# Kernel tuning notes

Measured on AMD Instinct MI355X. Metric: run time of the kernel, lower is better.

Reference implementation:

```python
import jax, jax.numpy as jnp
import numpy as np

V0 = 25; WIN = 3; NS = 6; EPS = 1e-5

def _build_scales():
    # ring graph on 25 joints (matches A_binary in init_kwargs)
    A = np.zeros((V0, V0), np.float32)
    for i in range(V0):
        A[i, (i + 1) % V0] = 1.0; A[(i + 1) % V0, i] = 1.0
    AL = np.tile(A + np.eye(V0, dtype=A.dtype), (WIN, WIN))  # spatial-temporal graph (75x75)
    I = np.eye(len(AL), dtype=AL.dtype)
    def shell(k):
        return np.minimum(np.linalg.matrix_power(AL + I, k), 1) - np.minimum(np.linalg.matrix_power(AL + I, k - 1), 1)
    def kadj(k):
        return I.copy() if k == 0 else shell(k) + I  # with_self=True
    def norm(g):
        dinv = np.power(g.sum(-1), -0.5)
        Dm = np.eye(len(g)) * dinv
        return (Dm @ g @ Dm).astype(np.float32)
    def klap(k):
        if k == 0:
            return I.astype(np.float32)
        Ak = shell(k)
        D = Ak.sum(-1)
        Dm = np.eye(len(D)) * np.power(D, -0.5)
        return (Dm @ (np.eye(len(D)) * (D + 2) - Ak) @ Dm).astype(np.float32)
    A_scales = np.concatenate([norm(kadj(k)) for k in range(NS)])  # (NS*75, 75)
    B_scales = np.concatenate([klap(k) for k in range(NS)])        # (NS*75, 75)
    return jnp.asarray(A_scales), jnp.asarray(B_scales)

def _bn(x, g, b):
    # BatchNorm2d in training mode: batch stats over (N, T, V)
    m = x.mean(axis=(0, 2, 3), keepdims=True)
    v = x.var(axis=(0, 2, 3), keepdims=True)
    return (x - m) * jax.lax.rsqrt(v + EPS) * g[None, :, None, None] + b[None, :, None, None]

def setup_inputs():
    key = jax.random.key(0)
    ks = jax.random.split(key, 4)
    N, C, T = 8, 96, 128
    A_scales, B_scales = _build_scales()
    d_in = C * NS * 2
    return {
        'x': jax.random.normal(ks[0], (N, C, T, V0), jnp.float32),
        'A_scales': A_scales,
        'B_scales': B_scales,
        'A_res': jax.random.uniform(ks[1], A_scales.shape, jnp.float32, -1e-6, 1e-6),
        'W_mlp': jax.random.normal(ks[2], (C, d_in), jnp.float32) / np.sqrt(d_in),
        'b_mlp': jnp.zeros((C,), jnp.float32),
        'g1': jnp.ones((C,), jnp.float32),
        'bt1': jnp.zeros((C,), jnp.float32),
        'W_out': jax.random.normal(ks[3], (C, C, WIN), jnp.float32) / np.sqrt(C * WIN),
        'b_out': jnp.zeros((C,), jnp.float32),
        'g2': jnp.ones((C,), jnp.float32),
        'bt2': jnp.zeros((C,), jnp.float32),
    }

def _forward(x, A_scales, B_scales, A_res, W_mlp, b_mlp, g1, bt1, W_out, b_out, g2, bt2):
    N, C, T, V = x.shape
    xp = jnp.pad(x, ((0, 0), (0, 0), (1, 1), (0, 0)))
    xu = jnp.stack([xp[:, :, w:w + T, :] for w in range(WIN)], axis=3).reshape(N, C, T, WIN * V)
    VL = WIN * V
    A = A_scales + A_res
    B = B_scales + A_res
    def agg(M):
        a = jnp.einsum('vu,nctu->nctv', M, xu)               # (N, C, T, NS*VL)
        a = a.reshape(N, C, T, NS, VL).transpose(0, 3, 1, 2, 4)
        return a.reshape(N, NS * C, T, VL)
    h = jnp.concatenate([agg(A), agg(B)], axis=1)            # (N, 2*NS*C, T, VL)
    # MLP: 1x1 conv -> ReLU -> BN
    h = jnp.einsum('oi,nitv->notv', W_mlp, h) + b_mlp[None, :, None, None]
    h = _bn(jax.nn.relu(h), g1, bt1)
    h = jax.nn.relu(h)                                       # gcn: act(mlp + residual(=0))
    h = h.reshape(N, C, T, WIN, V)
    out = jnp.einsum('oiw,nitwv->notv', W_out, h) + b_out[None, :, None, None]
    return _bn(out, g2, bt2)

def reference(x, A_scales, B_scales, A_res, W_mlp, b_mlp, g1, bt1, W_out, b_out, g2, bt2):
    return _forward(x, A_scales, B_scales, A_res, W_mlp, b_mlp, g1, bt1, W_out, b_out, g2, bt2)
```

## Files before the change

### kernel.cpp

```cpp
#include <hip/hip_runtime.h>


#define NB 8
#define CB 96
#define TB 128
#define VB 25
#define VLB 75
#define EPSB 1e-5f
#define XRS 104
#define TMS 104
#define HBS 296

typedef __attribute__((ext_vector_type(8))) short bf16x8;
typedef __attribute__((ext_vector_type(4))) float f32x4;

__device__ inline unsigned short f2bf(float f) {
  unsigned int u = __float_as_uint(f);
  u = (u + 0x7FFFu + ((u >> 16) & 1u)) >> 16;
  return (unsigned short)u;
}
__device__ inline float bf2f(unsigned short u) {
  return __uint_as_float(((unsigned int)u) << 16);
}

__global__ __launch_bounds__(256) void k0_init(
    const float* __restrict__ As, const float* __restrict__ Bs,
    const float* __restrict__ Ar, const float* __restrict__ Wm,
    const float* __restrict__ Wo,
    unsigned short* __restrict__ ABsw, unsigned short* __restrict__ Wsw,
    unsigned short* __restrict__ Wosw, float* __restrict__ stats) {
  int i = blockIdx.x * 256 + threadIdx.x;
  if (i < 110592) {
    int ps = i / 9216, r = i % 9216;
    int wv = r / 1536, r2 = r % 1536;
    int kk = r2 / 512, r3 = r2 % 512;
    int lane = r3 / 8, j = r3 % 8;
    int o = wv * 16 + (lane & 15);
    int c = kk * 32 + (lane >> 4) * 8 + j;
    Wsw[i] = f2bf(Wm[o * 1152 + ps * 96 + c]);
  }
  if (i < 92160) {
    int ps = i / 7680, r = i % 7680;
    int nt = r / 1536, r2 = r % 1536;
    int kk = r2 / 512, r3 = r2 % 512;
    int lane = r3 / 8, j = r3 % 8;
    int u = nt * 16 + (lane & 15);
    int up = kk * 32 + (lane >> 4) * 8 + j;
    float v = 0.f;
    if (u < 75 && up < 75) {
      int path = ps / 6, s = ps % 6;
      int idx = (s * 75 + u) * 75 + up;
      v = (path == 0 ? As[idx] : Bs[idx]) + Ar[idx];
    }
    ABsw[i] = f2bf(v);
  }
  if (i < 27648) {
    int wv = i / 4608, r = i % 4608;
    int kk = r / 512, r3 = r % 512;
    int lane = r3 / 8, j = r3 % 8;
    int o = wv * 16 + (lane & 15);
    int k = kk * 32 + (lane >> 4) * 8 + j;
    Wosw[i] = f2bf(Wo[o * 288 + k]);
  }
  if (i < 384) stats[i] = 0.f;
}

__global__ __launch_bounds__(384, 2) void k1t2(
    const float* __restrict__ x, const unsigned short* __restrict__ ABsw,
    const unsigned short* __restrict__ Wsw, const float* __restrict__ bm,
    unsigned short* __restrict__ h_relu, float* __restrict__ stats1) {
  __shared__ unsigned short xraw[112 * XRS];
  __shared__ unsigned short tmp_s[2][96 * TMS];
  __shared__ float st1s[96], st2s[96];
  const int tid = threadIdx.x;
  const int n = blockIdx.x >> 6, t0 = (blockIdx.x & 63) * 2;
  const int wave = tid >> 6, lane = tid & 63;
  const int l15 = lane & 15, quad = lane >> 4, q8 = quad * 8;
  const int wrow16 = wave * 16;

  for (int idx = tid; idx < 96 * 112; idx += 384) {
    int c = idx / 112, r = idx - c * 112;
    float v = 0.f;
    if (r < 100) {
      int tt = t0 - 1 + r / 25, vv = r % 25;
      if (tt >= 0 && tt < TB) v = x[((n * CB + c) * TB + tt) * VB + vv];
    }
    xraw[r * XRS + c] = f2bf(v);
  }
  for (int idx = tid; idx < 2 * 96 * 16; idx += 384) {
    int b = idx / (96 * 16), rem = idx - b * 96 * 16;
    tmp_s[b][(rem / 16) * TMS + 80 + rem % 16] = 0;
  }
  __syncthreads();

  const f32x4 zf = {0.f, 0.f, 0.f, 0.f};
  f32x4 acc2[2][5];
#pragma unroll
  for (int d = 0; d < 2; ++d)
#pragma unroll
    for (int nt = 0; nt < 5; ++nt) acc2[d][nt] = zf;

  const unsigned short* Wbase = Wsw + wave * 1536 + lane * 8;
  const unsigned short* Bbase = ABsw + lane * 8;

#pragma unroll
  for (int ps = 0; ps < 12; ++ps) {
    bf16x8 wa[3];
#pragma unroll
    for (int kk = 0; kk < 3; ++kk)
      wa[kk] = *reinterpret_cast<const bf16x8*>(Wbase + ps * 9216 + kk * 512);
    bf16x8 bf[15];
#pragma unroll
    for (int i = 0; i < 15; ++i)
      bf[i] = *reinterpret_cast<const bf16x8*>(Bbase + ps * 7680 + i * 512);

    f32x4 acc1[5];
#pragma unroll
    for (int nt = 0; nt < 5; ++nt) acc1[nt] = zf;
#pragma unroll
    for (int kk = 0; kk < 3; ++kk)
#pragma unroll
      for (int nt = 0; nt < 5; ++nt) {
        bf16x8 b = *reinterpret_cast<const bf16x8*>(&xraw[(nt * 16 + l15) * XRS + kk * 32 + q8]);
        acc1[nt] = __builtin_amdgcn_mfma_f32_16x16x32_bf16(wa[kk], b, acc1[nt], 0, 0, 0);
      }
#pragma unroll
    for (int nt = 0; nt < 5; ++nt) {
      int col = nt * 16 + l15;
#pragma unroll
      for (int r = 0; r < 4; ++r) {
        unsigned short v = (col < 75) ? f2bf(acc1[nt][r]) : (unsigned short)0;
        tmp_s[0][(wrow16 + quad * 4 + r) * TMS + col] = v;
      }
    }
#pragma unroll
    for (int nt = 0; nt < 5; ++nt) acc1[nt] = zf;
#pragma unroll
    for (int kk = 0; kk < 3; ++kk)
#pragma unroll
      for (int nt = 0; nt < 5; ++nt) {
        bf16x8 b = *reinterpret_cast<const bf16x8*>(&xraw[(25 + nt * 16 + l15) * XRS + kk * 32 + q8]);
        acc1[nt] = __builtin_amdgcn_mfma_f32_16x16x32_bf16(wa[kk], b, acc1[nt], 0, 0, 0);
      }
#pragma unroll
    for (int nt = 0; nt < 5; ++nt) {
      int col = nt * 16 + l15;
#pragma unroll
      for (int r = 0; r < 4; ++r) {
        unsigned short v = (col < 75) ? f2bf(acc1[nt][r]) : (unsigned short)0;
        tmp_s[1][(wrow16 + quad * 4 + r) * TMS + col] = v;
      }
    }

#pragma unroll
    for (int kk = 0; kk < 3; ++kk) {
      bf16x8 a0 = *reinterpret_cast<const bf16x8*>(&tmp_s[0][(wrow16 + l15) * TMS + kk * 32 + q8]);
#pragma unroll
      for (int nt = 0; nt < 5; ++nt)
        acc2[0][nt] = __builtin_amdgcn_mfma_f32_16x16x32_bf16(a0, bf[nt * 3 + kk], acc2[0][nt], 0, 0, 0);
      bf16x8 a1 = *reinterpret_cast<const bf16x8*>(&tmp_s[1][(wrow16 + l15) * TMS + kk * 32 + q8]);
#pragma unroll
      for (int nt = 0; nt < 5; ++nt)
        acc2[1][nt] = __builtin_amdgcn_mfma_f32_16x16x32_bf16(a1, bf[nt * 3 + kk], acc2[1][nt], 0, 0, 0);
    }
  }

  const int orow = wrow16 + quad * 4;
  float s1[4] = {0.f, 0.f, 0.f, 0.f}, s2[4] = {0.f, 0.f, 0.f, 0.f};
#pragma unroll
  for (int d = 0; d < 2; ++d) {
    const int t = t0 + d;
#pragma unroll
    for (int r = 0; r < 4; ++r) {
      const int o = orow + r;
      const float bias = bm[o];
      unsigned short* hp = h_relu + ((n * CB + o) * TB + t) * VLB;
#pragma unroll
      for (int nt = 0; nt < 5; ++nt) {
        int u = nt * 16 + l15;
        if (u < VLB) {
          float v = acc2[d][nt][r] + bias;
          v = v > 0.f ? v : 0.f;
          hp[u] = f2bf(v);
          s1[r] += v;
          s2[r] += v * v;
        }
      }
    }
  }
#pragma unroll
  for (int off = 1; off < 16; off <<= 1) {
#pragma unroll
    for (int r = 0; r < 4; ++r) {
      s1[r] += __shfl_xor(s1[r], off, 64);
      s2[r] += __shfl_xor(s2[r], off, 64);
    }
  }
  if (l15 == 0) {
#pragma unroll
    for (int r = 0; r < 4; ++r) { st1s[orow + r] = s1[r]; st2s[orow + r] = s2[r]; }
  }
  __syncthreads();
  if (tid < 96) {
    atomicAdd(&stats1[tid], st1s[tid]);
    atomicAdd(&stats1[96 + tid], st2s[tid]);
  }
}

__global__ __launch_bounds__(384) void k3n(
    const unsigned short* __restrict__ h_relu, const float* __restrict__ stats1,
    const float* __restrict__ g1, const float* __restrict__ bt1,
    const unsigned short* __restrict__ Wosw, const float* __restrict__ bo,
    float* __restrict__ out_pre, float* __restrict__ stats2) {
  __shared__ unsigned short hnb[2][32 * HBS];
  __shared__ float a1s[96], b1s[96];
  __shared__ float st1[96], st2[96];
  const int tid = threadIdx.x;
  const int n = blockIdx.x >> 6, t0 = (blockIdx.x & 63) * 2;

  if (tid < 96) {
    const float inv = 1.f / (8.f * 128.f * 75.f);
    float m = stats1[tid] * inv;
    float var = stats1[96 + tid] * inv - m * m;
    float a = g1[tid] * rsqrtf(var + EPSB);
    a1s[tid] = a;
    b1s[tid] = bt1[tid] - m * a;
  }
  for (int idx = tid; idx < 2 * 7 * HBS; idx += 384) {
    int d = idx / (7 * HBS), rm = idx % (7 * HBS);
    hnb[d][25 * HBS + rm] = 0;
  }
  __syncthreads();

  for (int idx = tid; idx < 2 * 96 * 75; idx += 384) {
    int d = idx / 7200, rm = idx % 7200;
    int i = rm / 75, u = rm - i * 75;
    float hv = bf2f(h_relu[((n * CB + i) * TB + t0 + d) * VLB + u]);
    float v = a1s[i] * hv + b1s[i];
    v = v > 0.f ? v : 0.f;
    int w = u / 25, vv = u - w * 25;
    hnb[d][vv * HBS + i * 3 + w] = f2bf(v);
  }
  __syncthreads();

  const int wave = tid >> 6, lane = tid & 63;
  const int l15 = lane & 15, quad = lane >> 4, q8 = quad * 8;
  const f32x4 zf = {0.f, 0.f, 0.f, 0.f};
  f32x4 acc[2][2] = {{zf, zf}, {zf, zf}};
  const unsigned short* Apw = Wosw + wave * 4608 + lane * 8;
#pragma unroll
  for (int kk = 0; kk < 9; ++kk) {
    bf16x8 a = *reinterpret_cast<const bf16x8*>(Apw + kk * 512);
#pragma unroll
    for (int d = 0; d < 2; ++d) {
      bf16x8 b0 = *reinterpret_cast<const bf16x8*>(&hnb[d][l15 * HBS + kk * 32 + q8]);
      bf16x8 b1 = *reinterpret_cast<const bf16x8*>(&hnb[d][(16 + l15) * HBS + kk * 32 + q8]);
      acc[d][0] = __builtin_amdgcn_mfma_f32_16x16x32_bf16(a, b0, acc[d][0], 0, 0, 0);
      acc[d][1] = __builtin_amdgcn_mfma_f32_16x16x32_bf16(a, b1, acc[d][1], 0, 0, 0);
    }
  }

  const int orow = wave * 16 + quad * 4;
  float s1[4] = {0.f, 0.f, 0.f, 0.f}, s2[4] = {0.f, 0.f, 0.f, 0.f};
#pragma unroll
  for (int d = 0; d < 2; ++d) {
#pragma unroll
    for (int nt = 0; nt < 2; ++nt) {
      int v = nt * 16 + l15;
      if (v < VB) {
#pragma unroll
        for (int r = 0; r < 4; ++r) {
          const int o = orow + r;
          float val = acc[d][nt][r] + bo[o];
          out_pre[((n * CB + o) * TB + t0 + d) * VB + v] = val;
          s1[r] += val;
          s2[r] += val * val;
        }
      }
    }
  }
#pragma unroll
  for (int off = 1; off < 16; off <<= 1) {
#pragma unroll
    for (int r = 0; r < 4; ++r) {
      s1[r] += __shfl_xor(s1[r], off, 64);
      s2[r] += __shfl_xor(s2[r], off, 64);
    }
  }
  if (l15 == 0) {
#pragma unroll
    for (int r = 0; r < 4; ++r) { st1[orow + r] = s1[r]; st2[orow + r] = s2[r]; }
  }
  __syncthreads();
  if (tid < 96) {
    atomicAdd(&stats2[tid], st1[tid]);
    atomicAdd(&stats2[96 + tid], st2[tid]);
  }
}

__global__ __launch_bounds__(256) void k5_bn2(
    const float* __restrict__ out_pre, const float* __restrict__ stats2,
    const float* __restrict__ g2, const float* __restrict__ bt2,
    float* __restrict__ out) {
  int idx = blockIdx.x * 256 + threadIdx.x;
  if (idx >= NB * CB * TB * VB / 4) return;
  int o = (idx / (TB * VB / 4)) % CB;
  const float inv = 1.f / (8.f * 128.f * 25.f);
  float m = stats2[o] * inv;
  float var = stats2[96 + o] * inv - m * m;
  float a = g2[o] * rsqrtf(var + EPSB);
  float b = bt2[o] - m * a;
  f32x4 vin = reinterpret_cast<const f32x4*>(out_pre)[idx];
  f32x4 vo;
#pragma unroll
  for (int j = 0; j < 4; ++j) vo[j] = a * vin[j] + b;
  reinterpret_cast<f32x4*>(out)[idx] = vo;
}

extern "C" void kernel_launch(void* const* d_in, const int* in_sizes, int n_in,
                              void* d_out, int out_size, void* d_ws, size_t ws_size,
                              hipStream_t stream) {
  const float* x   = (const float*)d_in[0];
  const float* As  = (const float*)d_in[1];
  const float* Bs  = (const float*)d_in[2];
  const float* Ar  = (const float*)d_in[3];
  const float* Wm  = (const float*)d_in[4];
  const float* bm  = (const float*)d_in[5];
  const float* g1  = (const float*)d_in[6];
  const float* bt1 = (const float*)d_in[7];
  const float* Wo  = (const float*)d_in[8];
  const float* bo  = (const float*)d_in[9];
  const float* g2  = (const float*)d_in[10];
  const float* bt2 = (const float*)d_in[11];
  float* out = (float*)d_out;

  char* base = (char*)d_ws;
  unsigned short* HR   = (unsigned short*)base;
  float* out_pre       = (float*)(base + 14745600);
  unsigned short* ABsw = (unsigned short*)(base + 24576000);
  unsigned short* Wsw  = (unsigned short*)(base + 24760320);
  unsigned short* Wosw = (unsigned short*)(base + 24981504);
  float* stats         = (float*)(base + 25036800);
  float* stats1 = stats, *stats2 = stats + 192;

  k0_init<<<432, 256, 0, stream>>>(As, Bs, Ar, Wm, Wo, ABsw, Wsw, Wosw, stats);
  k1t2<<<NB * TB / 2, 384, 0, stream>>>(x, ABsw, Wsw, bm, HR, stats1);
  k3n<<<NB * TB / 2, 384, 0, stream>>>(HR, stats1, g1, bt1, Wosw, bo, out_pre, stats2);
  k5_bn2<<<(NB * CB * TB * VB / 4 + 255) / 256, 256, 0, stream>>>(out_pre, stats2, g2, bt2, out);
}
```

Baseline: 191.2 us.

## Software-pipeline k1 operand loads, relayout h_relu per timestep, and split k3 per t

In k1, the next stage's weight and adjacency fragments are now prefetched while the current stage's second GEMM runs, and the first GEMM for the next stage is issued early. The col<75 masking is dropped and occupancy is raised to 3 blocks. The intermediate h_relu moves to a (N,T,C,VL) layout so k3 can read it with contiguous 16-byte vector loads. k3 now handles one timestep per block with twice as many blocks and requests 4 blocks per CU. The main risks are register pressure from the prefetched fragments under the tighter launch bound, and garbage in padded columns 75-79 now that the mask is gone.

```diff
diff --git a/kernel.cpp b/kernel.cpp
--- a/kernel.cpp
+++ b/kernel.cpp
@@ -65,7 +65,7 @@
   if (i < 384) stats[i] = 0.f;
 }
 
-__global__ __launch_bounds__(384, 2) void k1t2(
+__global__ __launch_bounds__(384, 3) void k1t2(
     const float* __restrict__ x, const unsigned short* __restrict__ ABsw,
     const unsigned short* __restrict__ Wsw, const float* __restrict__ bm,
     unsigned short* __restrict__ h_relu, float* __restrict__ stats1) {
@@ -103,17 +103,9 @@
   const unsigned short* Wbase = Wsw + wave * 1536 + lane * 8;
   const unsigned short* Bbase = ABsw + lane * 8;
 
-#pragma unroll
-  for (int ps = 0; ps < 12; ++ps) {
-    bf16x8 wa[3];
-#pragma unroll
-    for (int kk = 0; kk < 3; ++kk)
-      wa[kk] = *reinterpret_cast<const bf16x8*>(Wbase + ps * 9216 + kk * 512);
-    bf16x8 bf[15];
-#pragma unroll
-    for (int i = 0; i < 15; ++i)
-      bf[i] = *reinterpret_cast<const bf16x8*>(Bbase + ps * 7680 + i * 512);
-
+  bf16x8 wa[3], bfr[15];
+
+  auto g1both = [&]() {
     f32x4 acc1[5];
 #pragma unroll
     for (int nt = 0; nt < 5; ++nt) acc1[nt] = zf;
@@ -128,10 +120,8 @@
     for (int nt = 0; nt < 5; ++nt) {
       int col = nt * 16 + l15;
 #pragma unroll
-      for (int r = 0; r < 4; ++r) {
-        unsigned short v = (col < 75) ? f2bf(acc1[nt][r]) : (unsigned short)0;
-        tmp_s[0][(wrow16 + quad * 4 + r) * TMS + col] = v;
-      }
+      for (int r = 0; r < 4; ++r)
+        tmp_s[0][(wrow16 + quad * 4 + r) * TMS + col] = f2bf(acc1[nt][r]);
     }
 #pragma unroll
     for (int nt = 0; nt < 5; ++nt) acc1[nt] = zf;
@@ -146,22 +136,42 @@
     for (int nt = 0; nt < 5; ++nt) {
       int col = nt * 16 + l15;
 #pragma unroll
-      for (int r = 0; r < 4; ++r) {
-        unsigned short v = (col < 75) ? f2bf(acc1[nt][r]) : (unsigned short)0;
-        tmp_s[1][(wrow16 + quad * 4 + r) * TMS + col] = v;
-      }
-    }
-
+      for (int r = 0; r < 4; ++r)
+        tmp_s[1][(wrow16 + quad * 4 + r) * TMS + col] = f2bf(acc1[nt][r]);
+    }
+  };
+
+#pragma unroll
+  for (int kk = 0; kk < 3; ++kk)
+    wa[kk] = *reinterpret_cast<const bf16x8*>(Wbase + kk * 512);
+#pragma unroll
+  for (int i = 0; i < 15; ++i)
+    bfr[i] = *reinterpret_cast<const bf16x8*>(Bbase + i * 512);
+  g1both();
+
+#pragma unroll
+  for (int ps = 0; ps < 12; ++ps) {
+    if (ps < 11) {
+#pragma unroll
+      for (int kk = 0; kk < 3; ++kk)
+        wa[kk] = *reinterpret_cast<const bf16x8*>(Wbase + (ps + 1) * 9216 + kk * 512);
+    }
 #pragma unroll
     for (int kk = 0; kk < 3; ++kk) {
       bf16x8 a0 = *reinterpret_cast<const bf16x8*>(&tmp_s[0][(wrow16 + l15) * TMS + kk * 32 + q8]);
 #pragma unroll
       for (int nt = 0; nt < 5; ++nt)
-        acc2[0][nt] = __builtin_amdgcn_mfma_f32_16x16x32_bf16(a0, bf[nt * 3 + kk], acc2[0][nt], 0, 0, 0);
+        acc2[0][nt] = __builtin_amdgcn_mfma_f32_16x16x32_bf16(a0, bfr[nt * 3 + kk], acc2[0][nt], 0, 0, 0);
       bf16x8 a1 = *reinterpret_cast<const bf16x8*>(&tmp_s[1][(wrow16 + l15) * TMS + kk * 32 + q8]);
 #pragma unroll
       for (int nt = 0; nt < 5; ++nt)
-        acc2[1][nt] = __builtin_amdgcn_mfma_f32_16x16x32_bf16(a1, bf[nt * 3 + kk], acc2[1][nt], 0, 0, 0);
+        acc2[1][nt] = __builtin_amdgcn_mfma_f32_16x16x32_bf16(a1, bfr[nt * 3 + kk], acc2[1][nt], 0, 0, 0);
+    }
+    if (ps < 11) {
+#pragma unroll
+      for (int i = 0; i < 15; ++i)
+        bfr[i] = *reinterpret_cast<const bf16x8*>(Bbase + (ps + 1) * 7680 + i * 512);
+      g1both();
     }
   }
 
@@ -174,7 +184,7 @@
     for (int r = 0; r < 4; ++r) {
       const int o = orow + r;
       const float bias = bm[o];
-      unsigned short* hp = h_relu + ((n * CB + o) * TB + t) * VLB;
+      unsigned short* hp = h_relu + ((n * TB + t) * CB + o) * VLB;
 #pragma unroll
       for (int nt = 0; nt < 5; ++nt) {
         int u = nt * 16 + l15;
@@ -207,16 +217,16 @@
   }
 }
 
-__global__ __launch_bounds__(384) void k3n(
+__global__ __launch_bounds__(384, 4) void k3n(
     const unsigned short* __restrict__ h_relu, const float* __restrict__ stats1,
     const float* __restrict__ g1, const float* __restrict__ bt1,
     const unsigned short* __restrict__ Wosw, const float* __restrict__ bo,
     float* __restrict__ out_pre, float* __restrict__ stats2) {
-  __shared__ unsigned short hnb[2][32 * HBS];
+  __shared__ unsigned short hnb[32 * HBS];
   __shared__ float a1s[96], b1s[96];
   __shared__ float st1[96], st2[96];
   const int tid = threadIdx.x;
-  const int n = blockIdx.x >> 6, t0 = (blockIdx.x & 63) * 2;
+  const int n = blockIdx.x >> 7, t = blockIdx.x & 127;
 
   if (tid < 96) {
     const float inv = 1.f / (8.f * 128.f * 75.f);
@@ -226,56 +236,52 @@
     a1s[tid] = a;
     b1s[tid] = bt1[tid] - m * a;
   }
-  for (int idx = tid; idx < 2 * 7 * HBS; idx += 384) {
-    int d = idx / (7 * HBS), rm = idx % (7 * HBS);
-    hnb[d][25 * HBS + rm] = 0;
-  }
-  __syncthreads();
-
-  for (int idx = tid; idx < 2 * 96 * 75; idx += 384) {
-    int d = idx / 7200, rm = idx % 7200;
-    int i = rm / 75, u = rm - i * 75;
-    float hv = bf2f(h_relu[((n * CB + i) * TB + t0 + d) * VLB + u]);
-    float v = a1s[i] * hv + b1s[i];
-    v = v > 0.f ? v : 0.f;
-    int w = u / 25, vv = u - w * 25;
-    hnb[d][vv * HBS + i * 3 + w] = f2bf(v);
+  for (int idx = tid; idx < 7 * HBS; idx += 384) hnb[25 * HBS + idx] = 0;
+  __syncthreads();
+
+  const unsigned short* hp = h_relu + (n * TB + t) * (CB * VLB);
+  for (int i8 = tid; i8 < 900; i8 += 384) {
+    bf16x8 v = *reinterpret_cast<const bf16x8*>(hp + i8 * 8);
+    const int e = i8 * 8;
+#pragma unroll
+    for (int j = 0; j < 8; ++j) {
+      int ee = e + j;
+      int i = ee / 75, u = ee - i * 75;
+      float val = a1s[i] * bf2f((unsigned short)v[j]) + b1s[i];
+      val = val > 0.f ? val : 0.f;
+      int w = u / 25, vv = u - w * 25;
+      hnb[vv * HBS + i * 3 + w] = f2bf(val);
+    }
   }
   __syncthreads();
 
   const int wave = tid >> 6, lane = tid & 63;
   const int l15 = lane & 15, quad = lane >> 4, q8 = quad * 8;
   const f32x4 zf = {0.f, 0.f, 0.f, 0.f};
-  f32x4 acc[2][2] = {{zf, zf}, {zf, zf}};
+  f32x4 acc[2] = {zf, zf};
   const unsigned short* Apw = Wosw + wave * 4608 + lane * 8;
 #pragma unroll
   for (int kk = 0; kk < 9; ++kk) {
     bf16x8 a = *reinterpret_cast<const bf16x8*>(Apw + kk * 512);
-#pragma unroll
-    for (int d = 0; d < 2; ++d) {
-      bf16x8 b0 = *reinterpret_cast<const bf16x8*>(&hnb[d][l15 * HBS + kk * 32 + q8]);
-      bf16x8 b1 = *reinterpret_cast<const bf16x8*>(&hnb[d][(16 + l15) * HBS + kk * 32 + q8]);
-      acc[d][0] = __builtin_amdgcn_mfma_f32_16x16x32_bf16(a, b0, acc[d][0], 0, 0, 0);
-      acc[d][1] = __builtin_amdgcn_mfma_f32_16x16x32_bf16(a, b1, acc[d][1], 0, 0, 0);
-    }
+    bf16x8 b0 = *reinterpret_cast<const bf16x8*>(&hnb[l15 * HBS + kk * 32 + q8]);
+    bf16x8 b1 = *reinterpret_cast<const bf16x8*>(&hnb[(16 + l15) * HBS + kk * 32 + q8]);
+    acc[0] = __builtin_amdgcn_mfma_f32_16x16x32_bf16(a, b0, acc[0], 0, 0, 0);
+    acc[1] = __builtin_amdgcn_mfma_f32_16x16x32_bf16(a, b1, acc[1], 0, 0, 0);
   }
 
   const int orow = wave * 16 + quad * 4;
   float s1[4] = {0.f, 0.f, 0.f, 0.f}, s2[4] = {0.f, 0.f, 0.f, 0.f};
 #pragma unroll
-  for (int d = 0; d < 2; ++d) {
-#pragma unroll
-    for (int nt = 0; nt < 2; ++nt) {
-      int v = nt * 16 + l15;
-      if (v < VB) {
-#pragma unroll
-        for (int r = 0; r < 4; ++r) {
-          const int o = orow + r;
-          float val = acc[d][nt][r] + bo[o];
-          out_pre[((n * CB + o) * TB + t0 + d) * VB + v] = val;
-          s1[r] += val;
-          s2[r] += val * val;
-        }
+  for (int nt = 0; nt < 2; ++nt) {
+    int v = nt * 16 + l15;
+    if (v < VB) {
+#pragma unroll
+      for (int r = 0; r < 4; ++r) {
+        const int o = orow + r;
+        float val = acc[nt][r] + bo[o];
+        out_pre[((n * CB + o) * TB + t) * VB + v] = val;
+        s1[r] += val;
+        s2[r] += val * val;
       }
     }
   }
@@ -345,6 +351,6 @@
 
   k0_init<<<432, 256, 0, stream>>>(As, Bs, Ar, Wm, Wo, ABsw, Wsw, Wosw, stats);
   k1t2<<<NB * TB / 2, 384, 0, stream>>>(x, ABsw, Wsw, bm, HR, stats1);
-  k3n<<<NB * TB / 2, 384, 0, stream>>>(HR, stats1, g1, bt1, Wosw, bo, out_pre, stats2);
+  k3n<<<NB * TB, 384, 0, stream>>>(HR, stats1, g1, bt1, Wosw, bo, out_pre, stats2);
   k5_bn2<<<(NB * CB * TB * VB / 4 + 255) / 256, 256, 0, stream>>>(out_pre, stats2, g2, bt2, out);
 }
```

Result: slower. 295.1 us (+54.3%).
